# Optimization experiments

Measured on AMD Instinct MI355X. Metric: run time of the kernel, lower is better.

## Reference

```python
import jax, jax.numpy as jnp
from jax import lax
import numpy as np

B, T, F = 256, 2048, 12
EV_VOCAB, RS_VOCAB = 32, 8
EED, RED = 6, 3
H, K = 96, 3
D = F + EED + RED  # 21


def setup_inputs() -> dict:
    key = jax.random.key(0)
    ks = jax.random.split(key, 12)
    s = 0.05
    return {
        'seq': jax.random.normal(ks[0], (B, T, F), jnp.float32),
        'ev': jax.random.randint(ks[1], (B, T), 0, EV_VOCAB),
        'rs': jax.random.randint(ks[2], (B, T), 0, RS_VOCAB),
        'lengths': jax.random.randint(ks[3], (B,), 1, T + 1),  # valid lengths in [1, T]
        'event_emb': jax.random.normal(ks[4], (EV_VOCAB, EED), jnp.float32) * s,
        'result_emb': jax.random.normal(ks[5], (RS_VOCAB, RED), jnp.float32) * s,
        'W_ih': jax.random.normal(ks[6], (4 * H, D), jnp.float32) * s,
        'W_hh': jax.random.normal(ks[7], (4 * H, H), jnp.float32) * s,
        'b_ih': jnp.zeros((4 * H,), jnp.float32),
        'b_hh': jnp.zeros((4 * H,), jnp.float32),
        'W_mlp': jax.random.normal(ks[8], (H, H * K), jnp.float32) * s,
        'b_mlp': jnp.zeros((H,), jnp.float32),
        'W_fc': jax.random.normal(ks[9], (2, 2 * H), jnp.float32) * s,
        'b_fc': jnp.zeros((2,), jnp.float32),
    }


def reference(seq, ev, rs, lengths, event_emb, result_emb, W_ih, W_hh, b_ih, b_hh,
              W_mlp, b_mlp, W_fc, b_fc):
    # embed + concat -> [B,T,D]
    x = jnp.concatenate([seq, event_emb[ev], result_emb[rs]], axis=-1)
    xs = jnp.swapaxes(x, 0, 1)  # [T,B,D]
    ts = jnp.arange(T)
    b = b_ih + b_hh

    def step(carry, inp):
        h, c = carry
        x_t, t = inp
        gates = x_t @ W_ih.T + h @ W_hh.T + b  # [B,4H]
        i, f, g, o = jnp.split(gates, 4, axis=-1)  # PyTorch gate order i,f,g,o
        i = jax.nn.sigmoid(i); f = jax.nn.sigmoid(f)
        g = jnp.tanh(g); o = jax.nn.sigmoid(o)
        c_new = f * c + i * g
        h_new = o * jnp.tanh(c_new)
        m = (t < lengths)[:, None]  # packed-seq semantics: freeze state past length
        h = jnp.where(m, h_new, h)
        c = jnp.where(m, c_new, c)
        out = jnp.where(m, h_new, jnp.zeros_like(h_new))  # pad_packed zeros
        return (h, c), out

    h0 = jnp.zeros((B, H), x.dtype)
    (h_fin, _), outs = lax.scan(step, (h0, h0), (xs, ts))
    out_padded = jnp.swapaxes(outs, 0, 1)  # [B,T,H]

    # vectorized last-k gather (replaces torch Python loop)
    idx = lengths[:, None] - K + jnp.arange(K)  # [B,K]
    valid = idx >= 0
    gathered = jnp.take_along_axis(out_padded, jnp.clip(idx, 0)[:, :, None], axis=1)
    gathered = jnp.where(valid[:, :, None], gathered, jnp.zeros_like(gathered))
    lastk = gathered.reshape(B, K * H)

    h_lastk = jax.nn.relu(lastk @ W_mlp.T + b_mlp)
    h = jnp.concatenate([h_fin, h_lastk], axis=1)  # [B,2H]
    return h @ W_fc.T + b_fc  # [B,2]
```

## Files before the change

kernel.cpp:

```cpp
#include <hip/hip_runtime.h>

#define TT 2048
#define FF 12
#define HH 96
#define CH 128
#define SLC 20
#define XW  40
#define L2E 1.44269504088896340736f

__device__ __forceinline__ float fast_exp2(float x){ return __builtin_amdgcn_exp2f(x); }
__device__ __forceinline__ float fast_rcp(float x){ return __builtin_amdgcn_rcpf(x); }

#define DPPF(x, ctrl) __int_as_float(__builtin_amdgcn_update_dpp(0, __float_as_int(x), (ctrl), 0xF, 0xF, true))
#define QP_XOR1 0xB1
#define QP_XOR2 0x4E
#define SHL4    0x104
#define SHL8    0x108

__global__ __launch_bounds__(512, 2) void lstm_persist(
  const float* __restrict__ seq, const int* __restrict__ ev, const int* __restrict__ rsi,
  const int* __restrict__ len, const float* __restrict__ eemb, const float* __restrict__ remb,
  const float* __restrict__ W_ih, const float* __restrict__ W_hh,
  const float* __restrict__ b_ih, const float* __restrict__ b_hh,
  const float* __restrict__ W_mlp, const float* __restrict__ b_mlp,
  const float* __restrict__ W_fc, const float* __restrict__ b_fc,
  float* __restrict__ out)
{
  const int b   = blockIdx.x;
  const int tid = threadIdx.x;
  const int G   = tid >> 4;
  const int lu  = tid & 15;
  const int oct = lu >> 3;
  const int cs  = lu & 7;

  __shared__ __align__(16) float vv[2][8*SLC];
  __shared__ __align__(16) float xch[CH][XW];
  __shared__ __align__(16) float lastk[3*HH];
  __shared__ __align__(16) float et[192];
  __shared__ __align__(16) float rt[24];
  __shared__ __align__(16) float accs[192];
  __shared__ __align__(16) float h2[192];
  __shared__ int evb[CH];
  __shared__ int rsb[CH];

  float wh[6][16], bg[6], cK[6], cM[6], cB[6];
  #pragma unroll
  for (int j = 0; j < 6; ++j) {
    const int lr   = 6*oct + j;
    const int u_   = 3*G + (lr >> 2);
    const int gate = lr & 3;
    const int grow = gate*96 + u_;
    #pragma unroll
    for (int i = 0; i < 16; ++i) {
      const int col = 16*cs + i;
      wh[j][i] = (col < 96) ? W_hh[grow*96 + col]
               : ((col < 117) ? W_ih[grow*21 + (col-96)] : 0.f);
    }
    bg[j] = (cs == 0) ? (b_ih[grow] + b_hh[grow]) : 0.f;
    const bool t = (gate == 2);
    cK[j] = t ? (-2.f*L2E) : (-L2E);
    cM[j] = t ? 2.f : 1.f;
    cB[j] = t ? -1.f : 0.f;
  }
  const int un = 3*G + ((lu == 8) ? 2 : lu);

  for (int i = tid; i < 2*8*SLC; i += 512) ((float*)vv)[i]  = 0.f;
  for (int i = tid; i < CH*XW;   i += 512) ((float*)xch)[i] = 0.f;
  for (int i = tid; i < 3*HH;    i += 512) lastk[i] = 0.f;
  if (tid < 192) et[tid] = eemb[tid];
  if (tid < 24)  rt[tid] = remb[tid];
  __syncthreads();

  float c_state = 0.f;
  const int L = len[b];

  for (int t0 = 0; t0 < L; t0 += CH) {
    for (int i = tid; i < CH*FF; i += 512) {
      const int r = i / 12, c = i - r*12;
      xch[r][c] = seq[(size_t)b*(TT*FF) + (size_t)t0*FF + i];
    }
    if (tid < CH) {
      evb[tid] = ev [b*TT + t0 + tid];
      rsb[tid] = rsi[b*TT + t0 + tid];
    }
    __syncthreads();
    for (int i = tid; i < CH*9; i += 512) {
      const int r = i / 9, c = 12 + (i - r*9);
      const float val = (c < 18) ? et[evb[r]*6 + (c-12)] : rt[rsb[r]*3 + (c-18)];
      xch[r][(c < 16) ? c : (c + 4)] = val;
    }
    __syncthreads();

    const int nr = min(CH, L - t0);
    for (int r = 0; r < nr; ++r) {
      const int p = (t0 + r) & 1;
      const float* vp = (cs < 6) ? (vv[p] + SLC*cs) : (&xch[r][(cs-6)*SLC]);
      float hb[16];
      #pragma unroll
      for (int i = 0; i < 4; ++i) *(float4*)&hb[4*i] = ((const float4*)vp)[i];

      float S[6];
      #pragma unroll
      for (int j = 0; j < 6; ++j) {
        float a0 = bg[j], a1 = 0.f;
        #pragma unroll
        for (int i = 0; i < 8; ++i) {
          a0 = fmaf(wh[j][2*i],   hb[2*i],   a0);
          a1 = fmaf(wh[j][2*i+1], hb[2*i+1], a1);
        }
        S[j] = a0 + a1;
      }
      #pragma unroll
      for (int j = 0; j < 6; ++j) S[j] += DPPF(S[j], SHL4);
      #pragma unroll
      for (int j = 0; j < 6; ++j) S[j] += DPPF(S[j], QP_XOR1);
      #pragma unroll
      for (int j = 0; j < 6; ++j) S[j] += DPPF(S[j], QP_XOR2);
      float A[6];
      #pragma unroll
      for (int j = 0; j < 6; ++j) {
        const float e = fast_exp2(cK[j]*S[j]);
        A[j] = fmaf(cM[j], fast_rcp(1.f + e), cB[j]);
      }
      const float X0 = DPPF(A[0], SHL8);
      const float X1 = DPPF(A[1], SHL8);
      if ((lu == 0) | (lu == 1) | (lu == 8)) {
        const float i_ = (lu==1) ? A[4] : ((lu==8) ? A[2] : A[0]);
        const float f_ = (lu==1) ? A[5] : ((lu==8) ? A[3] : A[1]);
        const float g_ = (lu==1) ? X0   : ((lu==8) ? A[4] : A[2]);
        const float o_ = (lu==1) ? X1   : ((lu==8) ? A[5] : A[3]);
        c_state = fmaf(f_, c_state, i_*g_);
        const float e2 = fast_exp2((-2.f*L2E)*fabsf(c_state));
        const float th = copysignf((1.f - e2)*fast_rcp(1.f + e2), c_state);
        const float hn = o_ * th;
        vv[p^1][SLC*(un >> 4) + (un & 15)] = hn;
        const int kk = (t0 + r) + 3 - L;
        if (kk >= 0) lastk[kk*96 + un] = hn;
      }
      __syncthreads();
    }
  }

  if (tid < 192) {
    const int hh = tid / 96;
    const int m  = tid - hh*96;
    const float* wp = W_mlp + m*288 + hh*144;
    const float* xq = lastk + hh*144;
    float s = 0.f;
    #pragma unroll 8
    for (int i = 0; i < 144; ++i) s = fmaf(wp[i], xq[i], s);
    accs[tid] = s;
  }
  __syncthreads();
  if (tid < 96) {
    const float hl = accs[tid] + accs[96+tid] + b_mlp[tid];
    h2[96 + tid] = fmaxf(hl, 0.f);
    h2[tid] = vv[L & 1][SLC*(tid >> 4) + (tid & 15)];
  }
  __syncthreads();
  if (tid < 128) {
    const int o  = tid >> 6;
    const int ll = tid & 63;
    const float* wf = W_fc + o*192 + 3*ll;
    float s = fmaf(wf[0], h2[3*ll+0], fmaf(wf[1], h2[3*ll+1], wf[2]*h2[3*ll+2]));
    #pragma unroll
    for (int off = 32; off > 0; off >>= 1) s += __shfl_down(s, off);
    if (ll == 0) out[b*2 + o] = s + b_fc[o];
  }
}

extern "C" void kernel_launch(void* const* d_in, const int* in_sizes, int n_in,
                              void* d_out, int out_size, void* d_ws, size_t ws_size,
                              hipStream_t stream) {
  const float* seq   = (const float*)d_in[0];
  const int*   ev    = (const int*)  d_in[1];
  const int*   rsi   = (const int*)  d_in[2];
  const int*   len   = (const int*)  d_in[3];
  const float* eemb  = (const float*)d_in[4];
  const float* remb  = (const float*)d_in[5];
  const float* W_ih  = (const float*)d_in[6];
  const float* W_hh  = (const float*)d_in[7];
  const float* b_ih  = (const float*)d_in[8];
  const float* b_hh  = (const float*)d_in[9];
  const float* W_mlp = (const float*)d_in[10];
  const float* b_mlp = (const float*)d_in[11];
  const float* W_fc  = (const float*)d_in[12];
  const float* b_fc  = (const float*)d_in[13];

  hipLaunchKernelGGL(lstm_persist, dim3(256), dim3(512), 0, stream,
                     seq, ev, rsi, len, eemb, remb, W_ih, W_hh, b_ih, b_hh,
                     W_mlp, b_mlp, W_fc, b_fc, (float*)d_out);
}
```

Measured before the change: 1.455 ms.

## Batch 16 sequences per block and compute LSTM gates with bf16 MFMA

Replaces the one-sequence-per-block scalar FMA LSTM with a kernel where each block handles 16 batch rows. The gate matmul (W_hh and W_ih concatenated) runs on 16x16x32 bf16 MFMA instructions, with the weights held in registers as A fragments and the hidden state stored as bf16 in shared memory. The grid shrinks from 256 to 16 blocks, so the recurrence now advances to the longest length among the 16 sequences and uses far fewer CUs. The bf16 rounding of weights, inputs and hidden state also introduces precision risk.

```diff
diff --git a/kernel.cpp b/kernel.cpp
--- a/kernel.cpp
+++ b/kernel.cpp
@@ -2,22 +2,27 @@
 
 #define TT 2048
 #define FF 12
-#define HH 96
-#define CH 128
-#define SLC 20
-#define XW  40
+#define NB 16
+#define CHK 64
 #define L2E 1.44269504088896340736f
+
+typedef __attribute__((ext_vector_type(8))) short bf16x8;
+typedef __attribute__((ext_vector_type(4))) float f32x4;
 
 __device__ __forceinline__ float fast_exp2(float x){ return __builtin_amdgcn_exp2f(x); }
 __device__ __forceinline__ float fast_rcp(float x){ return __builtin_amdgcn_rcpf(x); }
-
-#define DPPF(x, ctrl) __int_as_float(__builtin_amdgcn_update_dpp(0, __float_as_int(x), (ctrl), 0xF, 0xF, true))
-#define QP_XOR1 0xB1
-#define QP_XOR2 0x4E
-#define SHL4    0x104
-#define SHL8    0x108
-
-__global__ __launch_bounds__(512, 2) void lstm_persist(
+__device__ __forceinline__ unsigned short f2b(float x){
+  unsigned u = __float_as_uint(x);
+  return (unsigned short)((u + 0x7FFFu + ((u>>16)&1u)) >> 16);
+}
+__device__ __forceinline__ float sigf(float z){
+  return fast_rcp(1.f + fast_exp2((-L2E)*z));
+}
+__device__ __forceinline__ float tanh2(float z){
+  return fmaf(2.f, fast_rcp(1.f + fast_exp2((-2.f*L2E)*z)), -1.f);
+}
+
+__global__ __launch_bounds__(512, 1) void lstm_mfma(
   const float* __restrict__ seq, const int* __restrict__ ev, const int* __restrict__ rsi,
   const int* __restrict__ len, const float* __restrict__ eemb, const float* __restrict__ remb,
   const float* __restrict__ W_ih, const float* __restrict__ W_hh,
@@ -26,146 +31,153 @@
   const float* __restrict__ W_fc, const float* __restrict__ b_fc,
   float* __restrict__ out)
 {
-  const int b   = blockIdx.x;
   const int tid = threadIdx.x;
-  const int G   = tid >> 4;
-  const int lu  = tid & 15;
-  const int oct = lu >> 3;
-  const int cs  = lu & 7;
-
-  __shared__ __align__(16) float vv[2][8*SLC];
-  __shared__ __align__(16) float xch[CH][XW];
-  __shared__ __align__(16) float lastk[3*HH];
+  const int wv  = tid >> 6;
+  const int l   = tid & 63;
+  const int lg  = l >> 4;
+  const int n   = l & 15;
+  const int b16 = blockIdx.x * NB;
+
+  __shared__ __align__(16) unsigned short vbuf[2][12][17][8];
+  __shared__ __align__(16) unsigned short xprep[CHK][4][16][8];
+  __shared__ __align__(16) float lastk[NB][3][96];
+  __shared__ __align__(16) float hfin[NB][96];
+  __shared__ __align__(16) float hlk[NB][96];
   __shared__ __align__(16) float et[192];
   __shared__ __align__(16) float rt[24];
-  __shared__ __align__(16) float accs[192];
-  __shared__ __align__(16) float h2[192];
-  __shared__ int evb[CH];
-  __shared__ int rsb[CH];
-
-  float wh[6][16], bg[6], cK[6], cM[6], cB[6];
-  #pragma unroll
-  for (int j = 0; j < 6; ++j) {
-    const int lr   = 6*oct + j;
-    const int u_   = 3*G + (lr >> 2);
-    const int gate = lr & 3;
-    const int grow = gate*96 + u_;
+  __shared__ int evs[NB][CHK];
+  __shared__ int rss[NB][CHK];
+
+  bf16x8 Afr[3][4];
+  #pragma unroll
+  for (int jt = 0; jt < 3; ++jt) {
+    const int mt = 3*wv + jt;
+    const int m  = 16*mt + n;
+    const int grow = (m & 3)*96 + (m >> 2);
     #pragma unroll
-    for (int i = 0; i < 16; ++i) {
-      const int col = 16*cs + i;
-      wh[j][i] = (col < 96) ? W_hh[grow*96 + col]
-               : ((col < 117) ? W_ih[grow*21 + (col-96)] : 0.f);
-    }
-    bg[j] = (cs == 0) ? (b_ih[grow] + b_hh[grow]) : 0.f;
-    const bool t = (gate == 2);
-    cK[j] = t ? (-2.f*L2E) : (-L2E);
-    cM[j] = t ? 2.f : 1.f;
-    cB[j] = t ? -1.f : 0.f;
-  }
-  const int un = 3*G + ((lu == 8) ? 2 : lu);
-
-  for (int i = tid; i < 2*8*SLC; i += 512) ((float*)vv)[i]  = 0.f;
-  for (int i = tid; i < CH*XW;   i += 512) ((float*)xch)[i] = 0.f;
-  for (int i = tid; i < 3*HH;    i += 512) lastk[i] = 0.f;
+    for (int kt = 0; kt < 4; ++kt) {
+      bf16x8 a;
+      #pragma unroll
+      for (int j = 0; j < 8; ++j) {
+        const int k = 32*kt + 8*lg + j;
+        const float w = (k < 96) ? W_hh[grow*96 + k]
+                      : ((k < 117) ? W_ih[grow*21 + (k-96)] : 0.f);
+        a[j] = (short)f2b(w);
+      }
+      Afr[jt][kt] = a;
+    }
+  }
+  float bias[3][4];
+  int   uns[3];
+  #pragma unroll
+  for (int jt = 0; jt < 3; ++jt) {
+    const int u = 4*(3*wv + jt) + lg;
+    uns[jt] = u;
+    #pragma unroll
+    for (int g = 0; g < 4; ++g) bias[jt][g] = b_ih[g*96 + u] + b_hh[g*96 + u];
+  }
+  const int Ln = len[b16 + n];
+  int maxL = 0;
+  #pragma unroll
+  for (int j = 0; j < NB; ++j) maxL = max(maxL, len[b16 + j]);
+
+  float c_reg[3] = {0.f, 0.f, 0.f};
+  float h_reg[3] = {0.f, 0.f, 0.f};
+
+  for (int i = tid; i < 2*12*17*8; i += 512) ((unsigned short*)vbuf)[i] = 0;
+  for (int i = tid; i < NB*3*96;   i += 512) ((float*)lastk)[i] = 0.f;
   if (tid < 192) et[tid] = eemb[tid];
   if (tid < 24)  rt[tid] = remb[tid];
-  __syncthreads();
-
-  float c_state = 0.f;
-  const int L = len[b];
-
-  for (int t0 = 0; t0 < L; t0 += CH) {
-    for (int i = tid; i < CH*FF; i += 512) {
-      const int r = i / 12, c = i - r*12;
-      xch[r][c] = seq[(size_t)b*(TT*FF) + (size_t)t0*FF + i];
-    }
-    if (tid < CH) {
-      evb[tid] = ev [b*TT + t0 + tid];
-      rsb[tid] = rsi[b*TT + t0 + tid];
+
+  for (int t0 = 0; t0 < maxL; t0 += CHK) {
+    for (int i = tid; i < NB*CHK; i += 512) {
+      const int nn = i >> 6, rr = i & (CHK-1);
+      evs[nn][rr] = ev [(b16+nn)*TT + t0 + rr];
+      rss[nn][rr] = rsi[(b16+nn)*TT + t0 + rr];
     }
     __syncthreads();
-    for (int i = tid; i < CH*9; i += 512) {
-      const int r = i / 9, c = 12 + (i - r*9);
-      const float val = (c < 18) ? et[evb[r]*6 + (c-12)] : rt[rsb[r]*3 + (c-18)];
-      xch[r][(c < 16) ? c : (c + 4)] = val;
+    for (int i = tid; i < CHK*512; i += 512) {
+      const int j  = i & 7;
+      const int n2 = (i >> 3) & 15;
+      const int g4 = (i >> 7) & 3;
+      const int r  = i >> 9;
+      const int c  = 8*g4 + j;
+      float v = 0.f;
+      if      (c < 12) v = seq[(size_t)(b16+n2)*(TT*FF) + (size_t)(t0+r)*FF + c];
+      else if (c < 18) v = et[evs[n2][r]*6 + (c-12)];
+      else if (c < 21) v = rt[rss[n2][r]*3 + (c-18)];
+      xprep[r][g4][n2][j] = f2b(v);
     }
     __syncthreads();
 
-    const int nr = min(CH, L - t0);
+    const int nr = min(CHK, maxL - t0);
     for (int r = 0; r < nr; ++r) {
       const int p = (t0 + r) & 1;
-      const float* vp = (cs < 6) ? (vv[p] + SLC*cs) : (&xch[r][(cs-6)*SLC]);
-      float hb[16];
+      bf16x8 B0 = *(const bf16x8*)&vbuf[p][lg    ][n][0];
+      bf16x8 B1 = *(const bf16x8*)&vbuf[p][4+lg  ][n][0];
+      bf16x8 B2 = *(const bf16x8*)&vbuf[p][8+lg  ][n][0];
+      bf16x8 B3 = *(const bf16x8*)&xprep[r][lg][n][0];
+      f32x4 acc[3];
       #pragma unroll
-      for (int i = 0; i < 4; ++i) *(float4*)&hb[4*i] = ((const float4*)vp)[i];
-
-      float S[6];
+      for (int jt = 0; jt < 3; ++jt) {
+        f32x4 a = {0.f, 0.f, 0.f, 0.f};
+        a = __builtin_amdgcn_mfma_f32_16x16x32_bf16(Afr[jt][0], B0, a, 0, 0, 0);
+        a = __builtin_amdgcn_mfma_f32_16x16x32_bf16(Afr[jt][1], B1, a, 0, 0, 0);
+        a = __builtin_amdgcn_mfma_f32_16x16x32_bf16(Afr[jt][2], B2, a, 0, 0, 0);
+        a = __builtin_amdgcn_mfma_f32_16x16x32_bf16(Afr[jt][3], B3, a, 0, 0, 0);
+        acc[jt] = a;
+      }
+      const int t = t0 + r;
+      const bool act = t < Ln;
       #pragma unroll
-      for (int j = 0; j < 6; ++j) {
-        float a0 = bg[j], a1 = 0.f;
-        #pragma unroll
-        for (int i = 0; i < 8; ++i) {
-          a0 = fmaf(wh[j][2*i],   hb[2*i],   a0);
-          a1 = fmaf(wh[j][2*i+1], hb[2*i+1], a1);
-        }
-        S[j] = a0 + a1;
-      }
-      #pragma unroll
-      for (int j = 0; j < 6; ++j) S[j] += DPPF(S[j], SHL4);
-      #pragma unroll
-      for (int j = 0; j < 6; ++j) S[j] += DPPF(S[j], QP_XOR1);
-      #pragma unroll
-      for (int j = 0; j < 6; ++j) S[j] += DPPF(S[j], QP_XOR2);
-      float A[6];
-      #pragma unroll
-      for (int j = 0; j < 6; ++j) {
-        const float e = fast_exp2(cK[j]*S[j]);
-        A[j] = fmaf(cM[j], fast_rcp(1.f + e), cB[j]);
-      }
-      const float X0 = DPPF(A[0], SHL8);
-      const float X1 = DPPF(A[1], SHL8);
-      if ((lu == 0) | (lu == 1) | (lu == 8)) {
-        const float i_ = (lu==1) ? A[4] : ((lu==8) ? A[2] : A[0]);
-        const float f_ = (lu==1) ? A[5] : ((lu==8) ? A[3] : A[1]);
-        const float g_ = (lu==1) ? X0   : ((lu==8) ? A[4] : A[2]);
-        const float o_ = (lu==1) ? X1   : ((lu==8) ? A[5] : A[3]);
-        c_state = fmaf(f_, c_state, i_*g_);
-        const float e2 = fast_exp2((-2.f*L2E)*fabsf(c_state));
-        const float th = copysignf((1.f - e2)*fast_rcp(1.f + e2), c_state);
-        const float hn = o_ * th;
-        vv[p^1][SLC*(un >> 4) + (un & 15)] = hn;
-        const int kk = (t0 + r) + 3 - L;
-        if (kk >= 0) lastk[kk*96 + un] = hn;
+      for (int jt = 0; jt < 3; ++jt) {
+        const float zi = acc[jt][0] + bias[jt][0];
+        const float zf = acc[jt][1] + bias[jt][1];
+        const float zg = acc[jt][2] + bias[jt][2];
+        const float zo = acc[jt][3] + bias[jt][3];
+        const float cn = fmaf(sigf(zf), c_reg[jt], sigf(zi)*tanh2(zg));
+        const float hn = sigf(zo) * tanh2(cn);
+        if (act) { c_reg[jt] = cn; h_reg[jt] = hn; }
+        const int u = uns[jt];
+        vbuf[p^1][u >> 3][n][u & 7] = f2b(h_reg[jt]);
+        const int kk = t + 3 - Ln;
+        if (kk >= 0 && kk < 3) lastk[n][kk][u] = hn;
       }
       __syncthreads();
     }
   }
 
-  if (tid < 192) {
-    const int hh = tid / 96;
-    const int m  = tid - hh*96;
-    const float* wp = W_mlp + m*288 + hh*144;
-    const float* xq = lastk + hh*144;
-    float s = 0.f;
-    #pragma unroll 8
-    for (int i = 0; i < 144; ++i) s = fmaf(wp[i], xq[i], s);
-    accs[tid] = s;
-  }
+  #pragma unroll
+  for (int jt = 0; jt < 3; ++jt) hfin[n][uns[jt]] = h_reg[jt];
   __syncthreads();
-  if (tid < 96) {
-    const float hl = accs[tid] + accs[96+tid] + b_mlp[tid];
-    h2[96 + tid] = fmaxf(hl, 0.f);
-    h2[tid] = vv[L & 1][SLC*(tid >> 4) + (tid & 15)];
+  {
+    const int ne = tid >> 5;
+    const int s  = tid & 31;
+    const float* lk = &lastk[ne][0][0];
+    for (int m = s; m < 96; m += 32) {
+      const float* wrow = W_mlp + m*288;
+      float a0 = 0.f, a1 = 0.f, a2 = 0.f;
+      #pragma unroll 4
+      for (int i = 0; i < 96; ++i) {
+        a0 = fmaf(wrow[i],       lk[i],       a0);
+        a1 = fmaf(wrow[96 + i],  lk[96 + i],  a1);
+        a2 = fmaf(wrow[192 + i], lk[192 + i], a2);
+      }
+      hlk[ne][m] = fmaxf((a0 + a1) + a2 + b_mlp[m], 0.f);
+    }
   }
   __syncthreads();
-  if (tid < 128) {
-    const int o  = tid >> 6;
-    const int ll = tid & 63;
-    const float* wf = W_fc + o*192 + 3*ll;
-    float s = fmaf(wf[0], h2[3*ll+0], fmaf(wf[1], h2[3*ll+1], wf[2]*h2[3*ll+2]));
-    #pragma unroll
-    for (int off = 32; off > 0; off >>= 1) s += __shfl_down(s, off);
-    if (ll == 0) out[b*2 + o] = s + b_fc[o];
+  if (tid < 32) {
+    const int ne = tid >> 1;
+    const int o  = tid & 1;
+    const float* wf = W_fc + o*192;
+    float a = b_fc[o];
+    #pragma unroll 4
+    for (int j = 0; j < 96; ++j) {
+      a = fmaf(wf[j],      hfin[ne][j], a);
+      a = fmaf(wf[96 + j], hlk[ne][j],  a);
+    }
+    out[(b16 + ne)*2 + o] = a;
   }
 }
 
@@ -187,7 +199,7 @@
   const float* W_fc  = (const float*)d_in[12];
   const float* b_fc  = (const float*)d_in[13];
 
-  hipLaunchKernelGGL(lstm_persist, dim3(256), dim3(512), 0, stream,
+  hipLaunchKernelGGL(lstm_mfma, dim3(16), dim3(512), 0, stream,
                      seq, ev, rsi, len, eemb, remb, W_ih, W_hh, b_ih, b_hh,
                      W_mlp, b_mlp, W_fc, b_fc, (float*)d_out);
 }
```

Result: slower. 2.163 ms (+48.7%).
